# Performance work log

Hardware: AMD Instinct MI355X
Metric: run time of the kernel (lower is better)

## Reference

```python
import jax, jax.numpy as jnp
import numpy as np
import math

N = 100000
E = 1600000
D = 256          # input_size
H = 64           # head_size = input_size // n_heads = 256 // 4


def setup_inputs() -> dict:
    key = jax.random.key(0)
    k1, k2, k3, k4, k5 = jax.random.split(key, 5)
    X = jax.random.normal(k1, (N, D), dtype=jnp.float32)
    edge_index = jax.random.randint(k2, (2, E), 0, N, dtype=jnp.int64)
    # Linear(input_size, head_size, bias=False) weights, stored as [D, H] so Q = X @ Wq
    s = 1.0 / math.sqrt(D)
    Wq = jax.random.uniform(k3, (D, H), dtype=jnp.float32, minval=-s, maxval=s)
    Wk = jax.random.uniform(k4, (D, H), dtype=jnp.float32, minval=-s, maxval=s)
    Wv = jax.random.uniform(k5, (D, H), dtype=jnp.float32, minval=-s, maxval=s)
    return {"X": X, "Wq": Wq, "Wk": Wk, "Wv": Wv, "edge_index": edge_index}


def reference(X, Wq, Wk, Wv, edge_index):
    dk = math.sqrt(H)
    Q = X @ Wq  # [N, H]
    K = X @ Wk
    V = X @ Wv
    src = edge_index[0]  # row of sparse matrix -> softmax segment (dim=1 softmax)
    dst = edge_index[1]  # column -> neighbor supplying K/V
    scores = jnp.sum(Q[src] * K[dst], axis=-1) / dk  # [E]
    # per-row (per src node) stable softmax over edges
    m = jax.ops.segment_max(scores, src, num_segments=N)          # [N], -inf for empty rows
    m = jnp.where(jnp.isfinite(m), m, 0.0)
    e = jnp.exp(scores - m[src])                                   # [E]
    denom = jax.ops.segment_sum(e, src, num_segments=N)            # [N]
    alpha = e / jnp.maximum(denom[src], 1e-38)                     # [E]
    # scatter-weighted V aggregation: out[i] = sum_{(i,j) in edges} alpha_ij * V[j]
    out = jax.ops.segment_sum(alpha[:, None] * V[dst], src, num_segments=N)  # [N, H]
    return out
```

## Files before the change

kernel.cpp:

```cpp
#include <hip/hip_runtime.h>

typedef unsigned short u16;
typedef unsigned int u32;
typedef short short8 __attribute__((ext_vector_type(8)));
typedef float f32x4 __attribute__((ext_vector_type(4)));
typedef u32 u32x4 __attribute__((ext_vector_type(4)));

__device__ __forceinline__ u16 f2bf(float f) {
    union { float f; u32 i; } c; c.f = f;
    u32 i = c.i;
    return (u16)((i + 0x7FFFu + ((i >> 16) & 1u)) >> 16);
}
__device__ __forceinline__ float bf2f(u16 u) {
    union { u32 i; float f; } c; c.i = ((u32)u) << 16; return c.f;
}
__device__ __forceinline__ void bf2x(u32 p, float& lo, float& hi) {
    union { u32 i; float f; } a, b;
    a.i = p << 16; b.i = p & 0xFFFF0000u;
    lo = a.f; hi = b.f;
}
__device__ __forceinline__ u32 cvtpk_bf16(float lo, float hi) {
    u32 r;
    asm("v_cvt_pk_bf16_f32 %0, %1, %2" : "=v"(r) : "v"(lo), "v"(hi));
    return r;
}

__global__ void wfrag_kernel(const float* __restrict__ Wq,
                             const float* __restrict__ Wk,
                             const float* __restrict__ Wv,
                             u16* __restrict__ wf)
{
    int idx = blockIdx.x * 256 + threadIdx.x;
    if (idx >= 12 * 8 * 64) return;
    int lane = idx & 63;
    int s = (idx >> 6) & 7;
    int t = idx >> 9;
    int n = t * 16 + (lane & 15);
    const float* Wsrc = (n < 64) ? Wq : ((n < 128) ? Wk : Wv);
    int col = n & 63;
    int kbase = s * 32 + (lane >> 4) * 8;
    u16 o[8];
#pragma unroll
    for (int j = 0; j < 8; ++j) o[j] = f2bf(Wsrc[(size_t)(kbase + j) * 64 + col]);
    *(short8*)(wf + (size_t)idx * 8) = *(const short8*)o;
}

#define TM 32
#define CB 320

__global__ __launch_bounds__(256, 3) void qkv_mfma(
    const float* __restrict__ X, const u16* __restrict__ wf,
    float* __restrict__ Qs, u16* __restrict__ KVsb,
    int N, int NT)
{
    __shared__ float xs[TM * 256];

    const int tid  = threadIdx.x;
    const int lane = tid & 63;
    const int wave = tid >> 6;
    const int m    = lane & 15;
    const int quad = lane >> 4;
    const int t0   = wave * 3;

    const short8* wfp = (const short8*)wf;
    short8 bfr0[8], bfr1[8], bfr2[8];
#pragma unroll
    for (int s = 0; s < 8; ++s) {
        bfr0[s] = wfp[(size_t)((t0 + 0) * 8 + s) * 64 + lane];
        bfr1[s] = wfp[(size_t)((t0 + 1) * 8 + s) * 64 + lane];
        bfr2[s] = wfp[(size_t)((t0 + 2) * 8 + s) * 64 + lane];
    }

    for (int tile = blockIdx.x; tile < NT; tile += gridDim.x) {
#pragma unroll
        for (int it = 0; it < 8; ++it) {
            int c0  = (it * 4 + wave) * 64;
            int c   = c0 + lane;
            int row = c >> 6;
            int sblk = (c & 63) ^ (row & 7);
            int arow = tile * TM + row;
            if (arow >= N) arow = N - 1;
            const float* g = X + (size_t)arow * 256 + sblk * 4;
            float* l = xs + c0 * 4;
            __builtin_amdgcn_global_load_lds(
                (const __attribute__((address_space(1))) void*)g,
                (__attribute__((address_space(3))) void*)l, 16, 0, 0);
        }
        __syncthreads();

        f32x4 acc[2][3];
#pragma unroll
        for (int rb = 0; rb < 2; ++rb)
#pragma unroll
            for (int tt = 0; tt < 3; ++tt) acc[rb][tt] = (f32x4)0.f;

#pragma unroll
        for (int rb = 0; rb < 2; ++rb) {
            const int row = rb * 16 + m;
            const float* xrow = xs + row * 256;
            const int sw = m & 7;
#pragma unroll
            for (int s = 0; s < 8; ++s) {
                int B0 = quad * 2 + s * 8;
                float4 a0 = *(const float4*)(xrow + ((B0)     ^ sw) * 4);
                float4 a1 = *(const float4*)(xrow + ((B0 + 1) ^ sw) * 4);
                union { u32x4 u; short8 s8; } af;
                af.u.x = cvtpk_bf16(a0.x, a0.y);
                af.u.y = cvtpk_bf16(a0.z, a0.w);
                af.u.z = cvtpk_bf16(a1.x, a1.y);
                af.u.w = cvtpk_bf16(a1.z, a1.w);
                acc[rb][0] = __builtin_amdgcn_mfma_f32_16x16x32_bf16(af.s8, bfr0[s], acc[rb][0], 0, 0, 0);
                acc[rb][1] = __builtin_amdgcn_mfma_f32_16x16x32_bf16(af.s8, bfr1[s], acc[rb][1], 0, 0, 0);
                acc[rb][2] = __builtin_amdgcn_mfma_f32_16x16x32_bf16(af.s8, bfr2[s], acc[rb][2], 0, 0, 0);
            }
        }

#pragma unroll
        for (int rb = 0; rb < 2; ++rb) {
            int rbase = tile * TM + rb * 16 + quad * 4;
#pragma unroll
            for (int tt = 0; tt < 3; ++tt) {
                int t = t0 + tt;
                int col = (t & 3) * 16 + m;
#pragma unroll
                for (int r = 0; r < 4; ++r) {
                    int rr = rbase + r;
                    if (rr >= N) continue;
                    float v = acc[rb][tt][r];
                    if (t < 4)      Qs  [(size_t)rr * 64  + col]      = v;
                    else if (t < 8) KVsb[(size_t)rr * 128 + col]      = f2bf(v);
                    else            KVsb[(size_t)rr * 128 + 64 + col] = f2bf(v);
                }
            }
        }
        __syncthreads();
    }
}

__global__ __launch_bounds__(256) void count_kernel(
    const int* __restrict__ src, int* __restrict__ bcnt,
    int E, int N, int NB, int chunk)
{
    __shared__ int cnt[512];
    for (int i = threadIdx.x; i < 512; i += 256) cnt[i] = 0;
    __syncthreads();
    int lo = blockIdx.x * chunk;
    int hi = min(E, lo + chunk);
    for (int e = lo + (int)threadIdx.x; e < hi; e += 256) {
        int s = src[e];
        if ((unsigned)s < (unsigned)N) atomicAdd(&cnt[s >> 8], 1);
    }
    __syncthreads();
    for (int b = threadIdx.x; b < NB; b += 256)
        bcnt[(size_t)b * CB + blockIdx.x] = cnt[b];
}

__global__ __launch_bounds__(256) void scatter_pairs_kernel(
    const int* __restrict__ src, const int* __restrict__ dst,
    const int* __restrict__ bcnt, u32* __restrict__ pairs,
    int* __restrict__ bbase, int* __restrict__ row_ptr_N,
    int E, int N, int NB, int chunk)
{
    __shared__ int basei[512];
    __shared__ int sc[512];
    __shared__ int cnt[512];

    const int blk = blockIdx.x;
    const int t = threadIdx.x;
    const int b0 = t, b1 = t + 256;

    int pre0 = 0, tot0 = 0, pre1 = 0, tot1 = 0;
    if (b0 < NB) {
        const int* r = bcnt + (size_t)b0 * CB;
        for (int i = 0; i < CB; ++i) {
            int v = r[i];
            tot0 += v;
            if (i < blk) pre0 += v;
        }
    }
    if (b1 < NB) {
        const int* r = bcnt + (size_t)b1 * CB;
        for (int i = 0; i < CB; ++i) {
            int v = r[i];
            tot1 += v;
            if (i < blk) pre1 += v;
        }
    }
    sc[t] = tot0;
    sc[t + 256] = tot1;
    __syncthreads();
    for (int off = 1; off < 512; off <<= 1) {
        int x0 = (t >= off) ? sc[t - off] : 0;
        int x1 = sc[t + 256 - off];
        __syncthreads();
        sc[t] += x0;
        sc[t + 256] += x1;
        __syncthreads();
    }
    if (b0 < NB) basei[b0] = (sc[t] - tot0) + pre0;
    if (b1 < NB) basei[b1] = (sc[t + 256] - tot1) + pre1;
    if (blk == 0) {
        if (b0 < NB) bbase[b0] = sc[t] - tot0;
        if (b1 < NB) bbase[b1] = sc[t + 256] - tot1;
        if (t == 255) {
            bbase[NB] = sc[511];
            *row_ptr_N = sc[511];
        }
    }
    for (int i = t; i < 512; i += 256) cnt[i] = 0;
    __syncthreads();

    int lo = blk * chunk;
    int hi = min(E, lo + chunk);
    for (int e = lo + t; e < hi; e += 256) {
        int s = src[e];
        if ((unsigned)s >= (unsigned)N) continue;
        int d = dst[e];
        if ((unsigned)d >= (unsigned)N) d = 0;
        int bk = s >> 8;
        int p = basei[bk] + atomicAdd(&cnt[bk], 1);
        pairs[p] = (u32)d | ((u32)(s & 255) << 24);
    }
}

#define MAXB 6144
__global__ __launch_bounds__(256) void sort_bucket_kernel(
    const u32* __restrict__ pairs, const int* __restrict__ bbase,
    int* __restrict__ row_ptr, int* __restrict__ sorted_dst, int N)
{
    __shared__ int deg[256];
    __shared__ int off[256];
    __shared__ int cur[256];
    __shared__ int ldst[MAXB];

    int bk = blockIdx.x;
    int n0 = bk * 256;
    int nn = min(256, N - n0);
    int base = bbase[bk];
    int size = bbase[bk + 1] - base;
    int t = threadIdx.x;

    deg[t] = 0;
    __syncthreads();
    for (int i = t; i < size; i += 256)
        atomicAdd(&deg[pairs[base + i] >> 24], 1);
    __syncthreads();
    off[t] = deg[t];
    __syncthreads();
    for (int s = 1; s < 256; s <<= 1) {
        int x = (t >= s) ? off[t - s] : 0;
        __syncthreads();
        off[t] += x;
        __syncthreads();
    }
    int excl = off[t] - deg[t];
    cur[t] = excl;
    if (t < nn) row_ptr[n0 + t] = base + excl;
    __syncthreads();
    int cap = min(size, MAXB);
    for (int i = t; i < size; i += 256) {
        u32 pr = pairs[base + i];
        int p = atomicAdd(&cur[pr >> 24], 1);
        if (p < MAXB) ldst[p] = (int)(pr & 0xFFFFFFu);
    }
    __syncthreads();
    for (int i = t; i < cap; i += 256)
        sorted_dst[base + i] = ldst[i];
    for (int i = cap + t; i < size; i += 256)
        sorted_dst[base + i] = 0;
}

__global__ __launch_bounds__(256) void attn_csr(
    const float* __restrict__ Qs, const u16* __restrict__ KVsb,
    const int* __restrict__ row_ptr, const int* __restrict__ sdst,
    float* __restrict__ out, int N)
{
    int sg = (int)((blockIdx.x * 256 + threadIdx.x) >> 3);
    if (sg >= N) return;
    int sl = threadIdx.x & 7;

    const float* qp = Qs + (size_t)sg * 64 + sl * 8;
    float4 q0 = *(const float4*)(qp);
    float4 q1 = *(const float4*)(qp + 4);

    int beg = row_ptr[sg];
    int end = row_ptr[sg + 1];

    float l = 0.f;
    float a0 = 0.f, a1 = 0.f, a2 = 0.f, a3 = 0.f;
    float a4 = 0.f, a5 = 0.f, a6 = 0.f, a7 = 0.f;

    if (beg < end) {
        const int last = end - 1;
        uint4 kr[4], vr[4];
        int pd[4];

#pragma unroll
        for (int i = 0; i < 4; ++i) {
            int e = beg + i;
            int d = sdst[e <= last ? e : last];
            const u16* kv = KVsb + (size_t)d * 128 + sl * 8;
            kr[i] = *(const uint4*)(kv);
            vr[i] = *(const uint4*)(kv + 64);
            int ep = beg + 4 + i;
            pd[i] = sdst[ep <= last ? ep : last];
        }

        for (int base = beg; base < end; base += 4) {
#pragma unroll
            for (int i = 0; i < 4; ++i) {
                int e = base + i;
                uint4 k = kr[i], v = vr[i];

                {
                    const u16* kv = KVsb + (size_t)pd[i] * 128 + sl * 8;
                    kr[i] = *(const uint4*)(kv);
                    vr[i] = *(const uint4*)(kv + 64);
                    int ep = e + 8;
                    pd[i] = sdst[ep <= last ? ep : last];
                }

                float k0, k1, k2, k3, k4, k5, k6, k7;
                bf2x(k.x, k0, k1); bf2x(k.y, k2, k3);
                bf2x(k.z, k4, k5); bf2x(k.w, k6, k7);

                float p = q0.x * k0 + q0.y * k1 + q0.z * k2 + q0.w * k3
                        + q1.x * k4 + q1.y * k5 + q1.z * k6 + q1.w * k7;
                p += __shfl_xor(p, 1);
                p += __shfl_xor(p, 2);
                p += __shfl_xor(p, 4);

                float pe = __expf(p * 0.125f);

                float v0, v1, v2, v3, v4, v5, v6, v7;
                bf2x(v.x, v0, v1); bf2x(v.y, v2, v3);
                bf2x(v.z, v4, v5); bf2x(v.w, v6, v7);

                if (e < end) {
                    l += pe;
                    a0 += pe * v0; a1 += pe * v1; a2 += pe * v2; a3 += pe * v3;
                    a4 += pe * v4; a5 += pe * v5; a6 += pe * v6; a7 += pe * v7;
                }
            }
        }
    }

    float inv = (l > 0.f) ? (1.f / l) : 0.f;
    float* op = out + (size_t)sg * 64 + sl * 8;
    *(float4*)(op)     = make_float4(a0 * inv, a1 * inv, a2 * inv, a3 * inv);
    *(float4*)(op + 4) = make_float4(a4 * inv, a5 * inv, a6 * inv, a7 * inv);
}

extern "C" void kernel_launch(void* const* d_in, const int* in_sizes, int n_in,
                              void* d_out, int out_size, void* d_ws, size_t ws_size,
                              hipStream_t stream)
{
    const float* X  = (const float*)d_in[0];
    const float* Wq = (const float*)d_in[1];
    const float* Wk = (const float*)d_in[2];
    const float* Wv = (const float*)d_in[3];
    const int*   ei = (const int*)d_in[4];

    const int N = in_sizes[0] / 256;
    const int E = in_sizes[4] / 2;
    const int* src = ei;
    const int* dst = ei + E;
    const int NB = (N + 255) >> 8;

    char* w = (char*)d_ws;
    float* Qs = (float*)w;      w += (size_t)N * 64 * sizeof(float);
    u16* KVsb = (u16*)w;        w += (size_t)N * 128 * sizeof(u16);
    u32* pairs = (u32*)w;       w += (size_t)E * sizeof(u32);
    int* sorted_dst = (int*)w;  w += (size_t)E * sizeof(int);
    int* row_ptr = (int*)w;     w += (size_t)(N + 1) * sizeof(int);
    int* bbase = (int*)w;       w += (size_t)(NB + 1) * sizeof(int);
    int* bcnt = (int*)w;        w += (size_t)NB * CB * sizeof(int);
    u16* wf = (u16*)w;          w += (size_t)12 * 8 * 64 * 8 * sizeof(u16);

    const int chunk = (E + CB - 1) / CB;
    const int NT = (N + TM - 1) / TM;

    wfrag_kernel<<<24, 256, 0, stream>>>(Wq, Wk, Wv, wf);
    qkv_mfma<<<768, 256, 0, stream>>>(X, wf, Qs, KVsb, N, NT);

    count_kernel<<<CB, 256, 0, stream>>>(src, bcnt, E, N, NB, chunk);
    scatter_pairs_kernel<<<CB, 256, 0, stream>>>(
        src, dst, bcnt, pairs, bbase, row_ptr + N, E, N, NB, chunk);
    sort_bucket_kernel<<<NB, 256, 0, stream>>>(
        pairs, bbase, row_ptr, sorted_dst, N);
    attn_csr<<<(N * 8 + 255) / 256, 256, 0, stream>>>(
        Qs, KVsb, row_ptr, sorted_dst, (float*)d_out, N);
}
```

Baseline: 328.1 us.

## Double-buffer X tiles in QKV MFMA kernel to overlap loads with compute

Adds a two-slot LDS buffer for X tiles so each block prefetches the next tile with global_load_lds while it runs MFMA on the current one. Synchronisation is now manual vmcnt waits plus raw s_barrier instead of __syncthreads, and the grid drops from 768 to 512 blocks with launch bounds lowered to 2 blocks per CU. This targets exposed global-load latency in the projection GEMM, at the cost of double the LDS per block and lower occupancy. The relaxed barriers may not order the LDS writes correctly.

```diff
diff --git a/kernel.cpp b/kernel.cpp
--- a/kernel.cpp
+++ b/kernel.cpp
@@ -47,13 +47,14 @@
 
 #define TM 32
 #define CB 320
-
-__global__ __launch_bounds__(256, 3) void qkv_mfma(
+#define QG 512
+
+__global__ __launch_bounds__(256, 2) void qkv_mfma(
     const float* __restrict__ X, const u16* __restrict__ wf,
     float* __restrict__ Qs, u16* __restrict__ KVsb,
     int N, int NT)
 {
-    __shared__ float xs[TM * 256];
+    __shared__ float xs[2][TM * 256];
 
     const int tid  = threadIdx.x;
     const int lane = tid & 63;
@@ -71,22 +72,38 @@
         bfr2[s] = wfp[(size_t)((t0 + 2) * 8 + s) * 64 + lane];
     }
 
-    for (int tile = blockIdx.x; tile < NT; tile += gridDim.x) {
-#pragma unroll
-        for (int it = 0; it < 8; ++it) {
-            int c0  = (it * 4 + wave) * 64;
-            int c   = c0 + lane;
-            int row = c >> 6;
-            int sblk = (c & 63) ^ (row & 7);
-            int arow = tile * TM + row;
-            if (arow >= N) arow = N - 1;
-            const float* g = X + (size_t)arow * 256 + sblk * 4;
-            float* l = xs + c0 * 4;
-            __builtin_amdgcn_global_load_lds(
-                (const __attribute__((address_space(1))) void*)g,
-                (__attribute__((address_space(3))) void*)l, 16, 0, 0);
-        }
-        __syncthreads();
+#define STAGE(BUF, TILE)                                                      \
+    {                                                                         \
+        _Pragma("unroll")                                                     \
+        for (int it = 0; it < 8; ++it) {                                      \
+            int c0  = (it * 4 + wave) * 64;                                   \
+            int c   = c0 + lane;                                              \
+            int row = c >> 6;                                                 \
+            int sblk = (c & 63) ^ (row & 7);                                  \
+            int arow = (TILE) * TM + row;                                     \
+            if (arow >= N) arow = N - 1;                                      \
+            const float* g = X + (size_t)arow * 256 + sblk * 4;               \
+            float* l = xs[BUF] + c0 * 4;                                      \
+            __builtin_amdgcn_global_load_lds(                                 \
+                (const __attribute__((address_space(1))) void*)g,             \
+                (__attribute__((address_space(3))) void*)l, 16, 0, 0);        \
+        }                                                                     \
+    }
+
+    if (blockIdx.x < NT) STAGE(0, blockIdx.x);
+
+    int k = 0;
+    for (int tile = blockIdx.x; tile < NT; tile += QG, ++k) {
+        const int cur = k & 1;
+        const int nxt = tile + QG;
+        if (nxt < NT) {
+            STAGE(cur ^ 1, nxt);
+            asm volatile("s_waitcnt vmcnt(8)" ::: "memory");
+        } else {
+            asm volatile("s_waitcnt vmcnt(0)" ::: "memory");
+        }
+        __builtin_amdgcn_sched_barrier(0);
+        __builtin_amdgcn_s_barrier();
 
         f32x4 acc[2][3];
 #pragma unroll
@@ -97,7 +114,7 @@
 #pragma unroll
         for (int rb = 0; rb < 2; ++rb) {
             const int row = rb * 16 + m;
-            const float* xrow = xs + row * 256;
+            const float* xrow = xs[cur] + row * 256;
             const int sw = m & 7;
 #pragma unroll
             for (int s = 0; s < 8; ++s) {
@@ -133,8 +150,9 @@
                 }
             }
         }
-        __syncthreads();
-    }
+        __builtin_amdgcn_s_barrier();
+    }
+#undef STAGE
 }
 
 __global__ __launch_bounds__(256) void count_kernel(
@@ -381,7 +399,7 @@
     const int NT = (N + TM - 1) / TM;
 
     wfrag_kernel<<<24, 256, 0, stream>>>(Wq, Wk, Wv, wf);
-    qkv_mfma<<<768, 256, 0, stream>>>(X, wf, Qs, KVsb, N, NT);
+    qkv_mfma<<<QG, 256, 0, stream>>>(X, wf, Qs, KVsb, N, NT);
 
     count_kernel<<<CB, 256, 0, stream>>>(src, bcnt, E, N, NB, chunk);
     scatter_pairs_kernel<<<CB, 256, 0, stream>>>(
```

Measured after the change: 314.3 us. 4.2% less time.
